# Kernel optimization log

Hardware: AMD Instinct MI355X
Metric: run time of the kernel (lower is better)

Reference implementation:

```python
import jax, jax.numpy as jnp
import numpy as np

D = 1024
H = 16

def setup_inputs() -> dict:
    key = jax.random.key(0)
    ks = jax.random.split(key, 5)
    x = jax.random.normal(ks[0], (2, 2048, D), dtype=jnp.float32)
    s = 0.02
    W_attn = jax.random.normal(ks[1], (D, 3 * D), dtype=jnp.float32) * s
    b_attn = jnp.zeros((3 * D,), dtype=jnp.float32)
    W_proj = jax.random.normal(ks[2], (D, D), dtype=jnp.float32) * s
    b_proj = jnp.zeros((D,), dtype=jnp.float32)
    return {"x": x, "W_attn": W_attn, "b_attn": b_attn, "W_proj": W_proj, "b_proj": b_proj}

def reference(x, W_attn, b_attn, W_proj, b_proj):
    B, S, E = x.shape
    hd = E // H  # head dim
    qkv = x @ W_attn + b_attn  # [B,S,3E]
    q, k, v = jnp.split(qkv, 3, axis=-1)
    # [B,S,E] -> [B,H,S,hd]
    q = q.reshape(B, S, H, hd).transpose(0, 2, 1, 3)
    k = k.reshape(B, S, H, hd).transpose(0, 2, 1, 3)
    v = v.reshape(B, S, H, hd).transpose(0, 2, 1, 3)
    att = jnp.einsum('bhqd,bhkd->bhqk', q, k) * (1.0 / jnp.sqrt(jnp.float32(hd)))
    causal = jnp.tril(jnp.ones((S, S), dtype=bool))
    att = jnp.where(causal, att, -jnp.inf)
    att = jax.nn.softmax(att, axis=-1)
    y = jnp.einsum('bhqk,bhkd->bhqd', att, v)
    y = y.transpose(0, 2, 1, 3).reshape(B, S, E)
    return y @ W_proj + b_proj
```

## Files before the change

kernel.cpp:

```cpp
#include <hip/hip_runtime.h>
#include <hip/hip_bf16.h>
#include <stdint.h>


typedef __attribute__((ext_vector_type(4))) float  f32x4;
typedef __attribute__((ext_vector_type(8))) __bf16 bf16x8;
typedef __attribute__((ext_vector_type(4))) short  s16x4;
typedef __attribute__((ext_vector_type(8))) short  s16x8;

#define MFMA(a, b, c) __builtin_amdgcn_mfma_f32_16x16x32_bf16((a), (b), (c), 0, 0, 0)

#if defined(__HIP_DEVICE_COMPILE__)
#define MFMA16(a, b, c) __builtin_amdgcn_mfma_f32_16x16x16bf16_1k((a), (b), (c), 0, 0, 0)
#else
#define MFMA16(a, b, c) (c)
#endif

__device__ __forceinline__ short f2bf(float x) {
#if defined(__HIP_DEVICE_COMPILE__)
  union { __bf16 b; short s; } u; u.b = (__bf16)x; return u.s;
#else
  union { float f; unsigned u; } v; v.f = x;
  unsigned r = v.u + 0x7FFFu + ((v.u >> 16) & 1u);
  return (short)(r >> 16);
#endif
}

__device__ __forceinline__ void gload16(const void* gptr, void* lptr) {
  __builtin_amdgcn_global_load_lds(
      (const __attribute__((address_space(1))) void*)gptr,
      (__attribute__((address_space(3))) void*)lptr, 16, 0, 0);
}


__global__ __launch_bounds__(256) void k_f32_to_bf16(const float* __restrict__ in,
                                                     short* __restrict__ out, int n) {
  int i = (blockIdx.x * 256 + threadIdx.x) * 4;
  if (i >= n) return;
  float4 v = *(const float4*)(in + i);
  s16x4 o;
  o[0] = f2bf(v.x); o[1] = f2bf(v.y); o[2] = f2bf(v.z); o[3] = f2bf(v.w);
  *(s16x4*)(out + i) = o;
}

__global__ __launch_bounds__(256) void k_transpose_bf(const float* __restrict__ W,
                                                      short* __restrict__ Wt, int R, int C) {
  __shared__ float tile[32][33];
  const int tx = threadIdx.x & 31, ty = threadIdx.x >> 5;
  const int bx = blockIdx.x * 32, by = blockIdx.y * 32;
#pragma unroll
  for (int i = 0; i < 4; ++i)
    tile[ty + i * 8][tx] = W[(long)(by + ty + i * 8) * C + bx + tx];
  __syncthreads();
#pragma unroll
  for (int i = 0; i < 4; ++i)
    Wt[(long)(bx + ty + i * 8) * R + by + tx] = f2bf(tile[tx][ty + i * 8]);
}


template <int EPI>
__global__ __launch_bounds__(256) void k_gemm(const short* __restrict__ A,
                                              const short* __restrict__ Bt,
                                              const float* __restrict__ bias,
                                              int M, int N, int K,
                                              short* __restrict__ q_out,
                                              short* __restrict__ k_out,
                                              short* __restrict__ vt_out,
                                              float* __restrict__ c_out) {
  __shared__ short As[3][4096];
  __shared__ short Bs[3][4096];
  const int tid  = threadIdx.x;
  const int lane = tid & 63;
  const int wave = tid >> 6;
  const int wm = (wave >> 1) * 64, wn = (wave & 1) * 64;
  const int bm = blockIdx.y * 128, bn = blockIdx.x * 128;
  const int sr = tid >> 2, sc = (tid & 3) * 8;
  const short* Ag = A + (long)(bm + sr) * K + sc;
  const short* Bg = Bt + (long)(bn + sr) * K + sc;
  const int fr = lane & 15, fg = lane >> 4;

  f32x4 acc[4][4];
#pragma unroll
  for (int i = 0; i < 4; ++i)
#pragma unroll
    for (int j = 0; j < 4; ++j) acc[i][j] = (f32x4){0.f, 0.f, 0.f, 0.f};

  auto stage = [&](int buf, int kt) {
    gload16(Ag + kt, &As[buf][tid * 8]);
    gload16(Ag + kt + 64 * K, &As[buf][2048 + tid * 8]);
    gload16(Bg + kt, &Bs[buf][tid * 8]);
    gload16(Bg + kt + 64 * K, &Bs[buf][2048 + tid * 8]);
  };
  auto compute = [&](int buf) {
    bf16x8 af[4], bfr[4];
    const short* Ar = &As[buf][(wm + fr) * 32 + fg * 8];
    const short* Br = &Bs[buf][(wn + fr) * 32 + fg * 8];
#pragma unroll
    for (int mi = 0; mi < 4; ++mi) af[mi] = *(const bf16x8*)(Ar + mi * 16 * 32);
#pragma unroll
    for (int ni = 0; ni < 4; ++ni) bfr[ni] = *(const bf16x8*)(Br + ni * 16 * 32);
#pragma unroll
    for (int mi = 0; mi < 4; ++mi)
#pragma unroll
      for (int ni = 0; ni < 4; ++ni)
        acc[mi][ni] = MFMA(af[mi], bfr[ni], acc[mi][ni]);
  };

  const int NT = K >> 5;
  stage(0, 0);
  stage(1, 32);
  for (int t = 0; t < NT - 1; ++t) {
    asm volatile("s_waitcnt vmcnt(4)" ::: "memory");
    __builtin_amdgcn_s_barrier();
    asm volatile("" ::: "memory");
    if (t + 2 < NT) stage((t + 2) % 3, (t + 2) << 5);
    compute(t % 3);
  }
  asm volatile("s_waitcnt vmcnt(0)" ::: "memory");
  __builtin_amdgcn_s_barrier();
  asm volatile("" ::: "memory");
  compute((NT - 1) % 3);

  const float QSC = 0.125f * 1.44269504088896341f;
#pragma unroll
  for (int mi = 0; mi < 4; ++mi) {
#pragma unroll
    for (int ni = 0; ni < 4; ++ni) {
      const int gcol  = bn + wn + ni * 16 + fr;
      const float bv  = bias[gcol];
      const int grow0 = bm + wm + mi * 16 + fg * 4;
      if (EPI == 0) {
        const int which = gcol >> 10;
        const int e = gcol & 1023;
        const int h = e >> 6, d = e & 63;
#pragma unroll
        for (int r = 0; r < 4; ++r) {
          const int mrow = grow0 + r;
          const int b = mrow >> 11, s = mrow & 2047;
          const float av = acc[mi][ni][r] + bv;
          if (which == 0)      q_out[((long)(b * 16 + h) * 2048 + s) * 64 + d] = f2bf(av * QSC);
          else if (which == 1) k_out[((long)(b * 16 + h) * 2048 + s) * 64 + d] = f2bf(av);
          else                 vt_out[((long)(b * 16 + h) * 64 + d) * 2048 + s] = f2bf(av);
        }
      } else {
#pragma unroll
        for (int r = 0; r < 4; ++r)
          c_out[(long)(grow0 + r) * N + gcol] = acc[mi][ni][r] + bv;
      }
    }
  }
}


__global__ __launch_bounds__(256, 4) void k_attn(const short* __restrict__ Qb,
                                                 const short* __restrict__ Kb,
                                                 const short* __restrict__ Vt,
                                                 short* __restrict__ Y) {
  __shared__ short smem[2][2][4096];
  const int bh = blockIdx.x;
  const int strip = 31 - blockIdx.y;
  const int qw0 = strip * 64;
  const int b = bh >> 4, h = bh & 15;
  const int tid = threadIdx.x;
  const int w = tid >> 6, lane = tid & 63;
  const int ql = lane & 15, g = lane >> 4;
  const short* Kp = Kb + (long)bh * 2048 * 64;
  const short* Vp = Vt + (long)bh * 64 * 2048;
  const short* Qp = Qb + ((long)bh * 2048 + qw0 + w * 16) * 64;

  const bf16x8 qf0 = *(const bf16x8*)(Qp + ql * 64 + g * 8);
  const bf16x8 qf1 = *(const bf16x8*)(Qp + ql * 64 + 32 + g * 8);

  const int sr_ = tid >> 3, sj_ = tid & 7;

  s16x4 ones;
  ones[0] = ones[1] = ones[2] = ones[3] = (short)0x3F80;

  f32x4 o[4];
#pragma unroll
  for (int df = 0; df < 4; ++df) o[df] = (f32x4){0.f, 0.f, 0.f, 0.f};
  f32x4 o_l = (f32x4){0.f, 0.f, 0.f, 0.f};
  float m = -1e30f;
  const int nt = strip + 1;

  {
#pragma unroll
    for (int j = 0; j < 2; ++j) {
      const int r = j * 32 + sr_;
      const int c = sj_ ^ (r & 7);
      gload16(Kp + (long)r * 64 + c * 8, &smem[0][0][j * 2048 + tid * 8]);
      gload16(Vp + (long)r * 2048 + c * 8, &smem[0][1][j * 2048 + tid * 8]);
    }
  }

  for (int t = 0; t < nt; ++t) {
    const int cur = t & 1;
    __syncthreads();
    if (t + 1 < nt) {
      const int k0n = (t + 1) * 64;
#pragma unroll
      for (int j = 0; j < 2; ++j) {
        const int r = j * 32 + sr_;
        const int c = sj_ ^ (r & 7);
        gload16(Kp + (long)(k0n + r) * 64 + c * 8, &smem[cur ^ 1][0][j * 2048 + tid * 8]);
        gload16(Vp + (long)r * 2048 + k0n + c * 8, &smem[cur ^ 1][1][j * 2048 + tid * 8]);
      }
    }
    const short* Kl = &smem[cur][0][0];
    const short* Vl = &smem[cur][1][0];
    const bool diag = (t == strip);

    float z[16];
    __builtin_amdgcn_s_setprio(1);
#pragma unroll
    for (int kf = 0; kf < 4; ++kf) {
      if (!diag || kf <= w) {
        const int r = kf * 16 + ql;
        const bf16x8 ka = *(const bf16x8*)(Kl + r * 64 + ((g ^ (r & 7)) * 8));
        const bf16x8 kb = *(const bf16x8*)(Kl + r * 64 + (((4 + g) ^ (r & 7)) * 8));
        f32x4 zz = (f32x4){0.f, 0.f, 0.f, 0.f};
        zz = MFMA(ka, qf0, zz);
        zz = MFMA(kb, qf1, zz);
        if (diag && kf == w) {
#pragma unroll
          for (int r4 = 0; r4 < 4; ++r4)
            z[kf * 4 + r4] = (g * 4 + r4 <= ql) ? zz[r4] : -3.0e38f;
        } else {
#pragma unroll
          for (int r4 = 0; r4 < 4; ++r4) z[kf * 4 + r4] = zz[r4];
        }
      } else {
#pragma unroll
        for (int r4 = 0; r4 < 4; ++r4) z[kf * 4 + r4] = -3.0e38f;
      }
    }
    __builtin_amdgcn_s_setprio(0);

    const float t1 = fmaxf(fmaxf(z[0], z[1]), z[2]);
    const float t2 = fmaxf(fmaxf(z[3], z[4]), z[5]);
    const float t3 = fmaxf(fmaxf(z[6], z[7]), z[8]);
    const float t4 = fmaxf(fmaxf(z[9], z[10]), z[11]);
    const float t5 = fmaxf(fmaxf(z[12], z[13]), z[14]);
    float tz = fmaxf(fmaxf(fmaxf(t1, t2), t3), fmaxf(fmaxf(t4, t5), z[15]));
    tz = fmaxf(tz, __shfl_xor(tz, 16));
    tz = fmaxf(tz, __shfl_xor(tz, 32));
    if (!__all(tz <= m + 8.0f)) {
      const float nm = fmaxf(m, tz);
      const float fac = exp2f(m - nm);
#pragma unroll
      for (int df = 0; df < 4; ++df) o[df] *= fac;
      o_l *= fac;
      m = nm;
    }
    __builtin_amdgcn_s_setprio(1);
#pragma unroll
    for (int kf = 0; kf < 4; ++kf) {
      if (!diag || kf <= w) {
        s16x4 pk;
        pk[0] = f2bf(exp2f(z[kf * 4 + 0] - m));
        pk[1] = f2bf(exp2f(z[kf * 4 + 1] - m));
        pk[2] = f2bf(exp2f(z[kf * 4 + 2] - m));
        pk[3] = f2bf(exp2f(z[kf * 4 + 3] - m));
        o_l = MFMA16(ones, pk, o_l);
#pragma unroll
        for (int df = 0; df < 4; ++df) {
          const int d = df * 16 + ql;
          const int c = kf * 2 + (g >> 1);
          const s16x4 vk = *(const s16x4*)(Vl + d * 64 + ((c ^ (d & 7)) * 8) + (g & 1) * 4);
          o[df] = MFMA16(vk, pk, o[df]);
        }
      }
    }
    __builtin_amdgcn_s_setprio(0);
  }

  __syncthreads();
  float* ot = (float*)&smem[0][0][0] + w * 1040;
  const float linv = 1.f / o_l[0];
#pragma unroll
  for (int df = 0; df < 4; ++df)
#pragma unroll
    for (int r = 0; r < 4; ++r)
      ot[ql * 65 + df * 16 + g * 4 + r] = o[df][r] * linv;
  const int q2 = lane >> 2, c4 = (lane & 3) * 16;
  short* Yp = Y + ((long)(b * 2048 + qw0 + w * 16 + q2)) * 1024 + h * 64 + c4;
  s16x8 y0, y1;
#pragma unroll
  for (int j = 0; j < 8; ++j) {
    y0[j] = f2bf(ot[q2 * 65 + c4 + j]);
    y1[j] = f2bf(ot[q2 * 65 + c4 + 8 + j]);
  }
  *(s16x8*)Yp = y0;
  *((s16x8*)(Yp + 8)) = y1;
}


extern "C" void kernel_launch(void* const* d_in, const int* in_sizes, int n_in,
                              void* d_out, int out_size, void* d_ws, size_t ws_size,
                              hipStream_t stream) {
  const float* x      = (const float*)d_in[0];
  const float* W_attn = (const float*)d_in[1];
  const float* b_attn = (const float*)d_in[2];
  const float* W_proj = (const float*)d_in[3];
  const float* b_proj = (const float*)d_in[4];
  float* out = (float*)d_out;

  char* ws = (char*)d_ws;
  short* x_bf = (short*)(ws);
  short* Wt_a = (short*)(ws + 8388608);
  short* Wt_p = (short*)(ws + 14680064);
  short* Qb   = (short*)(ws + 16777216);
  short* Kb   = (short*)(ws + 25165824);
  short* Vtb  = (short*)(ws + 33554432);
  short* y_bf = (short*)(ws + 41943040);

  k_f32_to_bf16<<<4096, 256, 0, stream>>>(x, x_bf, 4194304);
  k_transpose_bf<<<dim3(96, 32), 256, 0, stream>>>(W_attn, Wt_a, 1024, 3072);
  k_transpose_bf<<<dim3(32, 32), 256, 0, stream>>>(W_proj, Wt_p, 1024, 1024);
  k_gemm<0><<<dim3(24, 32), 256, 0, stream>>>(x_bf, Wt_a, b_attn, 4096, 3072, 1024,
                                              Qb, Kb, Vtb, nullptr);
  k_attn<<<dim3(32, 32), 256, 0, stream>>>(Qb, Kb, Vtb, y_bf);
  k_gemm<1><<<dim3(8, 32), 256, 0, stream>>>(y_bf, Wt_p, b_proj, 4096, 1024, 1024,
                                             nullptr, nullptr, nullptr, out);
}
```

Baseline: 127.7 us.

## Add 256x256-tile 8-wave QKV GEMM with phased double-buffered loads

Replaces the generic 128x128 QKV projection GEMM with a dedicated kernel that uses 256x256 tiles, 512 threads (8 waves), and a double-buffered LDS pipeline. Each 64-wide K step is split into four phases that interleave the next tile's half-loads with MFMA compute and raise wave priority around the MFMAs. The aim is more operand reuse per LDS byte and better overlap of global loads with compute. The cost is only 192 blocks, which may underfill the CUs, plus more registers and LDS per block. The output projection keeps the old kernel under a new name.

```diff
diff --git a/kernel.cpp b/kernel.cpp
--- a/kernel.cpp
+++ b/kernel.cpp
@@ -58,15 +58,118 @@
 }
 
 
-template <int EPI>
-__global__ __launch_bounds__(256) void k_gemm(const short* __restrict__ A,
-                                              const short* __restrict__ Bt,
-                                              const float* __restrict__ bias,
-                                              int M, int N, int K,
-                                              short* __restrict__ q_out,
-                                              short* __restrict__ k_out,
-                                              short* __restrict__ vt_out,
-                                              float* __restrict__ c_out) {
+#define QKV_PHASE(PH, KK, MIH, TAILVM)                                        \
+  {                                                                           \
+    if (t + 1 < NT) {                                                         \
+      stage_half(nxt, (PH), (t + 1) << 6);                                    \
+      asm volatile("s_waitcnt vmcnt(6)" ::: "memory");                        \
+    } else {                                                                  \
+      asm volatile("s_waitcnt vmcnt(" TAILVM ")" ::: "memory");               \
+    }                                                                         \
+    __builtin_amdgcn_s_barrier();                                             \
+    {                                                                         \
+      const short* Ab = &Als[cur][(KK) * 8192 + (wr * 128 + (MIH) * 64 + fr) * 32 + fg * 8]; \
+      if ((MIH) == 0) {                                                       \
+        const short* Bb = &Bls[cur][(KK) * 8192 + (wc * 64 + fr) * 32 + fg * 8]; \
+        _Pragma("unroll")                                                     \
+        for (int ni = 0; ni < 4; ++ni) bfr[ni] = *(const bf16x8*)(Bb + ni * 512); \
+      }                                                                       \
+      bf16x8 af[4];                                                           \
+      _Pragma("unroll")                                                       \
+      for (int mi = 0; mi < 4; ++mi) af[mi] = *(const bf16x8*)(Ab + mi * 512); \
+      __builtin_amdgcn_s_setprio(1);                                          \
+      _Pragma("unroll")                                                       \
+      for (int mi = 0; mi < 4; ++mi)                                          \
+        _Pragma("unroll")                                                     \
+        for (int ni = 0; ni < 4; ++ni)                                        \
+          acc[(MIH) * 4 + mi][ni] = MFMA(af[mi], bfr[ni], acc[(MIH) * 4 + mi][ni]); \
+      __builtin_amdgcn_s_setprio(0);                                          \
+    }                                                                         \
+  }
+
+__global__ __launch_bounds__(512, 2) void k_gemm_qkv(const short* __restrict__ A,
+                                                     const short* __restrict__ Bt,
+                                                     const float* __restrict__ bias,
+                                                     short* __restrict__ q_out,
+                                                     short* __restrict__ k_out,
+                                                     short* __restrict__ vt_out) {
+  constexpr int K = 1024;
+  constexpr int NT = 16;
+  __shared__ short Als[2][16384];
+  __shared__ short Bls[2][16384];
+  const int tid = threadIdx.x;
+  const int lane = tid & 63;
+  const int w = tid >> 6;
+  const int wr = w >> 2, wc = w & 3;
+  const int bm = blockIdx.y * 256, bn = blockIdx.x * 256;
+  const int fr = lane & 15, fg = lane >> 4;
+  const short* Ag = A + (long)(bm + (tid >> 2)) * K + (tid & 3) * 8;
+  const short* Bg = Bt + (long)(bn + (tid >> 2)) * K + (tid & 3) * 8;
+
+  f32x4 acc[8][4];
+#pragma unroll
+  for (int i = 0; i < 8; ++i)
+#pragma unroll
+    for (int j = 0; j < 4; ++j) acc[i][j] = (f32x4){0.f, 0.f, 0.f, 0.f};
+
+  auto stage_half = [&](int buf, int p, int kt) {
+    const int kk = p >> 1;
+    const int off = kt + kk * 32;
+    if (p & 1) {
+      short* dst = &Bls[buf][kk * 8192 + tid * 8];
+      gload16(Bg + off, dst);
+      gload16(Bg + 128 * K + off, dst + 4096);
+    } else {
+      short* dst = &Als[buf][kk * 8192 + tid * 8];
+      gload16(Ag + off, dst);
+      gload16(Ag + 128 * K + off, dst + 4096);
+    }
+  };
+
+  stage_half(0, 0, 0);
+  stage_half(0, 1, 0);
+  stage_half(0, 2, 0);
+  stage_half(0, 3, 0);
+
+  bf16x8 bfr[4];
+  for (int t = 0; t < NT; ++t) {
+    const int cur = t & 1, nxt = cur ^ 1;
+    QKV_PHASE(0, 0, 0, "6")
+    QKV_PHASE(1, 0, 1, "4")
+    QKV_PHASE(2, 1, 0, "2")
+    QKV_PHASE(3, 1, 1, "0")
+  }
+
+  const float QSC = 0.125f * 1.44269504088896341f;
+  const int which = bn >> 10;
+#pragma unroll
+  for (int mi = 0; mi < 8; ++mi) {
+#pragma unroll
+    for (int ni = 0; ni < 4; ++ni) {
+      const int gcol = bn + wc * 64 + ni * 16 + fr;
+      const float bv = bias[gcol];
+      const int grow0 = bm + wr * 128 + mi * 16 + fg * 4;
+      const int e = gcol & 1023;
+      const int h = e >> 6, d = e & 63;
+#pragma unroll
+      for (int r = 0; r < 4; ++r) {
+        const int mrow = grow0 + r;
+        const int b = mrow >> 11, s = mrow & 2047;
+        const float av = acc[mi][ni][r] + bv;
+        if (which == 0)      q_out[((long)(b * 16 + h) * 2048 + s) * 64 + d] = f2bf(av * QSC);
+        else if (which == 1) k_out[((long)(b * 16 + h) * 2048 + s) * 64 + d] = f2bf(av);
+        else                 vt_out[((long)(b * 16 + h) * 64 + d) * 2048 + s] = f2bf(av);
+      }
+    }
+  }
+}
+
+
+__global__ __launch_bounds__(256) void k_gemm_proj(const short* __restrict__ A,
+                                                   const short* __restrict__ Bt,
+                                                   const float* __restrict__ bias,
+                                                   int M, int N, int K,
+                                                   float* __restrict__ c_out) {
   __shared__ short As[3][4096];
   __shared__ short Bs[3][4096];
   const int tid  = threadIdx.x;
@@ -121,7 +224,6 @@
   asm volatile("" ::: "memory");
   compute((NT - 1) % 3);
 
-  const float QSC = 0.125f * 1.44269504088896341f;
 #pragma unroll
   for (int mi = 0; mi < 4; ++mi) {
 #pragma unroll
@@ -129,24 +231,9 @@
       const int gcol  = bn + wn + ni * 16 + fr;
       const float bv  = bias[gcol];
       const int grow0 = bm + wm + mi * 16 + fg * 4;
-      if (EPI == 0) {
-        const int which = gcol >> 10;
-        const int e = gcol & 1023;
-        const int h = e >> 6, d = e & 63;
-#pragma unroll
-        for (int r = 0; r < 4; ++r) {
-          const int mrow = grow0 + r;
-          const int b = mrow >> 11, s = mrow & 2047;
-          const float av = acc[mi][ni][r] + bv;
-          if (which == 0)      q_out[((long)(b * 16 + h) * 2048 + s) * 64 + d] = f2bf(av * QSC);
-          else if (which == 1) k_out[((long)(b * 16 + h) * 2048 + s) * 64 + d] = f2bf(av);
-          else                 vt_out[((long)(b * 16 + h) * 64 + d) * 2048 + s] = f2bf(av);
-        }
-      } else {
-#pragma unroll
-        for (int r = 0; r < 4; ++r)
-          c_out[(long)(grow0 + r) * N + gcol] = acc[mi][ni][r] + bv;
-      }
+#pragma unroll
+      for (int r = 0; r < 4; ++r)
+        c_out[(long)(grow0 + r) * N + gcol] = acc[mi][ni][r] + bv;
     }
   }
 }
@@ -317,9 +404,7 @@
   k_f32_to_bf16<<<4096, 256, 0, stream>>>(x, x_bf, 4194304);
   k_transpose_bf<<<dim3(96, 32), 256, 0, stream>>>(W_attn, Wt_a, 1024, 3072);
   k_transpose_bf<<<dim3(32, 32), 256, 0, stream>>>(W_proj, Wt_p, 1024, 1024);
-  k_gemm<0><<<dim3(24, 32), 256, 0, stream>>>(x_bf, Wt_a, b_attn, 4096, 3072, 1024,
-                                              Qb, Kb, Vtb, nullptr);
+  k_gemm_qkv<<<dim3(12, 16), 512, 0, stream>>>(x_bf, Wt_a, b_attn, Qb, Kb, Vtb);
   k_attn<<<dim3(32, 32), 256, 0, stream>>>(Qb, Kb, Vtb, y_bf);
-  k_gemm<1><<<dim3(8, 32), 256, 0, stream>>>(y_bf, Wt_p, b_proj, 4096, 1024, 1024,
-                                             nullptr, nullptr, nullptr, out);
-}
+  k_gemm_proj<<<dim3(8, 32), 256, 0, stream>>>(y_bf, Wt_p, b_proj, 4096, 1024, 1024, out);
+}
```

Result: slower. 145.6 us (+14.0%).

## Replace QKV GEMM with 256x256-tile 8-wave kernel using swizzled LDS

Applied to the files above, without the earlier changes.

The QKV projection moves from a 128x128-tile, 4-wave, triple-buffered GEMM to a dedicated 256x256-tile kernel with 8 waves and 64-wide K steps. It uses XOR-swizzled LDS layouts, double buffering with staggered A/B prefetch interleaved into the compute phases, and s_setprio around the MFMA bursts. The larger tile increases operand reuse per LDS load. In exchange it launches only 192 blocks, fewer than the 256 CUs, so it risks low occupancy and tail underuse, and the extra barriers per K step may add stalls.

```diff
diff --git a/kernel.cpp b/kernel.cpp
--- a/kernel.cpp
+++ b/kernel.cpp
@@ -58,15 +58,120 @@
 }
 
 
-template <int EPI>
-__global__ __launch_bounds__(256) void k_gemm(const short* __restrict__ A,
-                                              const short* __restrict__ Bt,
-                                              const float* __restrict__ bias,
-                                              int M, int N, int K,
-                                              short* __restrict__ q_out,
-                                              short* __restrict__ k_out,
-                                              short* __restrict__ vt_out,
-                                              float* __restrict__ c_out) {
+#define QKV_COMPUTE(KK, MIH, DOSTAGE)                                          \
+  {                                                                            \
+    if ((MIH) == 0) {                                                          \
+      _Pragma("unroll")                                                        \
+      for (int ni = 0; ni < 4; ++ni) {                                         \
+        const int row = wc * 64 + ni * 16 + fr;                                \
+        bfr[ni] = *(const bf16x8*)&Bls[cur][row * 64 + ((((KK)*4 + fg) ^ (fr & 7)) * 8)]; \
+      }                                                                        \
+    }                                                                          \
+    bf16x8 af[4];                                                              \
+    _Pragma("unroll")                                                          \
+    for (int mi = 0; mi < 4; ++mi) {                                           \
+      const int row = wr * 128 + (MIH) * 64 + mi * 16 + fr;                    \
+      af[mi] = *(const bf16x8*)&Als[cur][row * 64 + ((((KK)*4 + fg) ^ (fr & 7)) * 8)]; \
+    }                                                                          \
+    DOSTAGE;                                                                   \
+    __builtin_amdgcn_s_setprio(1);                                             \
+    _Pragma("unroll")                                                          \
+    for (int mi = 0; mi < 4; ++mi)                                             \
+      _Pragma("unroll")                                                        \
+      for (int ni = 0; ni < 4; ++ni)                                           \
+        acc[(MIH)*4 + mi][ni] = MFMA(af[mi], bfr[ni], acc[(MIH)*4 + mi][ni]);  \
+    __builtin_amdgcn_s_setprio(0);                                             \
+  }
+
+__global__ __launch_bounds__(512, 1) void k_gemm_qkv(const short* __restrict__ A,
+                                                     const short* __restrict__ Bt,
+                                                     const float* __restrict__ bias,
+                                                     short* __restrict__ q_out,
+                                                     short* __restrict__ k_out,
+                                                     short* __restrict__ vt_out) {
+  constexpr int K = 1024;
+  constexpr int NT = 16;
+  __shared__ short Als[2][16384];
+  __shared__ short Bls[2][16384];
+  const int tid = threadIdx.x;
+  const int lane = tid & 63;
+  const int w = tid >> 6;
+  const int wr = w >> 2, wc = w & 3;
+  const int bm = blockIdx.y * 256, bn = blockIdx.x * 256;
+  const int fr = lane & 15, fg = lane >> 4;
+
+  const int rt = tid >> 3;
+  const int csw = ((tid & 7) ^ (rt & 7)) * 8;
+  const short* Agb = A + (long)(bm + rt) * K + csw;
+  const short* Bgb = Bt + (long)(bn + rt) * K + csw;
+
+  f32x4 acc[8][4];
+#pragma unroll
+  for (int i = 0; i < 8; ++i)
+#pragma unroll
+    for (int j = 0; j < 4; ++j) acc[i][j] = (f32x4){0.f, 0.f, 0.f, 0.f};
+
+  auto stageA = [&](int buf, int t1) {
+    const long kt = (long)t1 << 6;
+#pragma unroll
+    for (int q = 0; q < 4; ++q)
+      gload16(Agb + kt + (long)q * (64 * K), &Als[buf][q * 4096 + tid * 8]);
+  };
+  auto stageB = [&](int buf, int t1) {
+    const long kt = (long)t1 << 6;
+#pragma unroll
+    for (int q = 0; q < 4; ++q)
+      gload16(Bgb + kt + (long)q * (64 * K), &Bls[buf][q * 4096 + tid * 8]);
+  };
+
+  stageA(0, 0);
+  stageB(0, 0);
+
+  bf16x8 bfr[4];
+  for (int t = 0; t < NT; ++t) {
+    const int cur = t & 1, nxt = cur ^ 1;
+    const bool pre = (t + 1 < NT);
+    asm volatile("s_waitcnt vmcnt(0)" ::: "memory");
+    __builtin_amdgcn_s_barrier();
+    QKV_COMPUTE(0, 0, { if (pre) stageA(nxt, t + 1); })
+    __builtin_amdgcn_s_barrier();
+    QKV_COMPUTE(0, 1, {})
+    __builtin_amdgcn_s_barrier();
+    QKV_COMPUTE(1, 0, { if (pre) stageB(nxt, t + 1); })
+    __builtin_amdgcn_s_barrier();
+    QKV_COMPUTE(1, 1, {})
+  }
+
+  const float QSC = 0.125f * 1.44269504088896341f;
+  const int which = bn >> 10;
+#pragma unroll
+  for (int mi = 0; mi < 8; ++mi) {
+#pragma unroll
+    for (int ni = 0; ni < 4; ++ni) {
+      const int gcol = bn + wc * 64 + ni * 16 + fr;
+      const float bv = bias[gcol];
+      const int grow0 = bm + wr * 128 + mi * 16 + fg * 4;
+      const int e = gcol & 1023;
+      const int h = e >> 6, d = e & 63;
+#pragma unroll
+      for (int r = 0; r < 4; ++r) {
+        const int mrow = grow0 + r;
+        const int b = mrow >> 11, s = mrow & 2047;
+        const float av = acc[mi][ni][r] + bv;
+        if (which == 0)      q_out[((long)(b * 16 + h) * 2048 + s) * 64 + d] = f2bf(av * QSC);
+        else if (which == 1) k_out[((long)(b * 16 + h) * 2048 + s) * 64 + d] = f2bf(av);
+        else                 vt_out[((long)(b * 16 + h) * 64 + d) * 2048 + s] = f2bf(av);
+      }
+    }
+  }
+}
+
+
+__global__ __launch_bounds__(256) void k_gemm_proj(const short* __restrict__ A,
+                                                   const short* __restrict__ Bt,
+                                                   const float* __restrict__ bias,
+                                                   int M, int N, int K,
+                                                   float* __restrict__ c_out) {
   __shared__ short As[3][4096];
   __shared__ short Bs[3][4096];
   const int tid  = threadIdx.x;
@@ -121,7 +226,6 @@
   asm volatile("" ::: "memory");
   compute((NT - 1) % 3);
 
-  const float QSC = 0.125f * 1.44269504088896341f;
 #pragma unroll
   for (int mi = 0; mi < 4; ++mi) {
 #pragma unroll
@@ -129,24 +233,9 @@
       const int gcol  = bn + wn + ni * 16 + fr;
       const float bv  = bias[gcol];
       const int grow0 = bm + wm + mi * 16 + fg * 4;
-      if (EPI == 0) {
-        const int which = gcol >> 10;
-        const int e = gcol & 1023;
-        const int h = e >> 6, d = e & 63;
-#pragma unroll
-        for (int r = 0; r < 4; ++r) {
-          const int mrow = grow0 + r;
-          const int b = mrow >> 11, s = mrow & 2047;
-          const float av = acc[mi][ni][r] + bv;
-          if (which == 0)      q_out[((long)(b * 16 + h) * 2048 + s) * 64 + d] = f2bf(av * QSC);
-          else if (which == 1) k_out[((long)(b * 16 + h) * 2048 + s) * 64 + d] = f2bf(av);
-          else                 vt_out[((long)(b * 16 + h) * 64 + d) * 2048 + s] = f2bf(av);
-        }
-      } else {
-#pragma unroll
-        for (int r = 0; r < 4; ++r)
-          c_out[(long)(grow0 + r) * N + gcol] = acc[mi][ni][r] + bv;
-      }
+#pragma unroll
+      for (int r = 0; r < 4; ++r)
+        c_out[(long)(grow0 + r) * N + gcol] = acc[mi][ni][r] + bv;
     }
   }
 }
@@ -317,9 +406,7 @@
   k_f32_to_bf16<<<4096, 256, 0, stream>>>(x, x_bf, 4194304);
   k_transpose_bf<<<dim3(96, 32), 256, 0, stream>>>(W_attn, Wt_a, 1024, 3072);
   k_transpose_bf<<<dim3(32, 32), 256, 0, stream>>>(W_proj, Wt_p, 1024, 1024);
-  k_gemm<0><<<dim3(24, 32), 256, 0, stream>>>(x_bf, Wt_a, b_attn, 4096, 3072, 1024,
-                                              Qb, Kb, Vtb, nullptr);
+  k_gemm_qkv<<<dim3(12, 16), 512, 0, stream>>>(x_bf, Wt_a, b_attn, Qb, Kb, Vtb);
   k_attn<<<dim3(32, 32), 256, 0, stream>>>(Qb, Kb, Vtb, y_bf);
-  k_gemm<1><<<dim3(8, 32), 256, 0, stream>>>(y_bf, Wt_p, b_proj, 4096, 1024, 1024,
-                                             nullptr, nullptr, nullptr, out);
-}
+  k_gemm_proj<<<dim3(8, 32), 256, 0, stream>>>(y_bf, Wt_p, b_proj, 4096, 1024, 1024, out);
+}
```

New measurement: 143.5 us. 1.12x slower.

## Process two 16-row query blocks per wave in attention; fuse prep kernels

Applied to the files above, without the earlier changes.

Each attention wave now handles 32 query rows (two 16-row groups) instead of 16, so each K/V tile loaded into LDS is reused across a 128-row strip and the grid shrinks to 32x16 blocks. Causal masking is generalized per sub-block using diagonal offsets, and occupancy is relaxed to 2 blocks per SM to allow more registers. Separately, the bf16 conversion of x and the two weight transposes are merged into one launch to cut launch overhead. The trade-offs are higher register pressure, fewer blocks in flight, and a coarser causal load imbalance.

```diff
diff --git a/kernel.cpp b/kernel.cpp
--- a/kernel.cpp
+++ b/kernel.cpp
@@ -33,21 +33,33 @@
 }
 
 
-__global__ __launch_bounds__(256) void k_f32_to_bf16(const float* __restrict__ in,
-                                                     short* __restrict__ out, int n) {
-  int i = (blockIdx.x * 256 + threadIdx.x) * 4;
-  if (i >= n) return;
-  float4 v = *(const float4*)(in + i);
-  s16x4 o;
-  o[0] = f2bf(v.x); o[1] = f2bf(v.y); o[2] = f2bf(v.z); o[3] = f2bf(v.w);
-  *(s16x4*)(out + i) = o;
-}
-
-__global__ __launch_bounds__(256) void k_transpose_bf(const float* __restrict__ W,
-                                                      short* __restrict__ Wt, int R, int C) {
+__global__ __launch_bounds__(256) void k_prep(const float* __restrict__ x,
+                                              const float* __restrict__ Wa,
+                                              const float* __restrict__ Wp,
+                                              short* __restrict__ x_bf,
+                                              short* __restrict__ Wt_a,
+                                              short* __restrict__ Wt_p) {
   __shared__ float tile[32][33];
+  const int id = blockIdx.x;
+  if (id < 4096) {
+    const int i = (id * 256 + threadIdx.x) * 4;
+    float4 v = *(const float4*)(x + i);
+    s16x4 o;
+    o[0] = f2bf(v.x); o[1] = f2bf(v.y); o[2] = f2bf(v.z); o[3] = f2bf(v.w);
+    *(s16x4*)(x_bf + i) = o;
+    return;
+  }
+  const float* W; short* Wt; int R, C, bx, by;
+  if (id < 7168) {
+    const int id2 = id - 4096;
+    W = Wa; Wt = Wt_a; R = 1024; C = 3072;
+    bx = (id2 % 96) * 32; by = (id2 / 96) * 32;
+  } else {
+    const int id2 = id - 7168;
+    W = Wp; Wt = Wt_p; R = 1024; C = 1024;
+    bx = (id2 & 31) * 32; by = (id2 >> 5) * 32;
+  }
   const int tx = threadIdx.x & 31, ty = threadIdx.x >> 5;
-  const int bx = blockIdx.x * 32, by = blockIdx.y * 32;
 #pragma unroll
   for (int i = 0; i < 4; ++i)
     tile[ty + i * 8][tx] = W[(long)(by + ty + i * 8) * C + bx + tx];
@@ -152,36 +164,39 @@
 }
 
 
-__global__ __launch_bounds__(256, 4) void k_attn(const short* __restrict__ Qb,
+__global__ __launch_bounds__(256, 2) void k_attn(const short* __restrict__ Qb,
                                                  const short* __restrict__ Kb,
                                                  const short* __restrict__ Vt,
                                                  short* __restrict__ Y) {
   __shared__ short smem[2][2][4096];
   const int bh = blockIdx.x;
-  const int strip = 31 - blockIdx.y;
-  const int qw0 = strip * 64;
+  const int strip = 15 - blockIdx.y;
+  const int qw0 = strip * 128;
   const int b = bh >> 4, h = bh & 15;
   const int tid = threadIdx.x;
   const int w = tid >> 6, lane = tid & 63;
   const int ql = lane & 15, g = lane >> 4;
   const short* Kp = Kb + (long)bh * 2048 * 64;
   const short* Vp = Vt + (long)bh * 64 * 2048;
-  const short* Qp = Qb + ((long)bh * 2048 + qw0 + w * 16) * 64;
-
-  const bf16x8 qf0 = *(const bf16x8*)(Qp + ql * 64 + g * 8);
-  const bf16x8 qf1 = *(const bf16x8*)(Qp + ql * 64 + 32 + g * 8);
+  const int qb0 = qw0 + w * 32;
+  const short* Qp = Qb + ((long)bh * 2048 + qb0) * 64;
+
+  const bf16x8 qf0a = *(const bf16x8*)(Qp + ql * 64 + g * 8);
+  const bf16x8 qf0b = *(const bf16x8*)(Qp + ql * 64 + 32 + g * 8);
+  const bf16x8 qf1a = *(const bf16x8*)(Qp + (16 + ql) * 64 + g * 8);
+  const bf16x8 qf1b = *(const bf16x8*)(Qp + (16 + ql) * 64 + 32 + g * 8);
 
   const int sr_ = tid >> 3, sj_ = tid & 7;
 
   s16x4 ones;
   ones[0] = ones[1] = ones[2] = ones[3] = (short)0x3F80;
 
-  f32x4 o[4];
-#pragma unroll
-  for (int df = 0; df < 4; ++df) o[df] = (f32x4){0.f, 0.f, 0.f, 0.f};
-  f32x4 o_l = (f32x4){0.f, 0.f, 0.f, 0.f};
-  float m = -1e30f;
-  const int nt = strip + 1;
+  f32x4 o0[4], o1[4];
+#pragma unroll
+  for (int df = 0; df < 4; ++df) { o0[df] = (f32x4){0.f,0.f,0.f,0.f}; o1[df] = (f32x4){0.f,0.f,0.f,0.f}; }
+  f32x4 ol0 = (f32x4){0.f,0.f,0.f,0.f}, ol1 = (f32x4){0.f,0.f,0.f,0.f};
+  float m0 = -1e30f, m1 = -1e30f;
+  const int nt = 2 * strip + 2;
 
   {
 #pragma unroll
@@ -208,66 +223,101 @@
     }
     const short* Kl = &smem[cur][0][0];
     const short* Vl = &smem[cur][1][0];
-    const bool diag = (t == strip);
-
-    float z[16];
+    const int k0 = t * 64;
+    const int dq0 = (qb0 - k0) >> 4;
+    const int dq1 = dq0 + 1;
+
+    float z0[16], z1[16];
+#pragma unroll
+    for (int j = 0; j < 16; ++j) { z0[j] = -3.0e38f; z1[j] = -3.0e38f; }
     __builtin_amdgcn_s_setprio(1);
 #pragma unroll
     for (int kf = 0; kf < 4; ++kf) {
-      if (!diag || kf <= w) {
+      if (kf <= dq1) {
         const int r = kf * 16 + ql;
         const bf16x8 ka = *(const bf16x8*)(Kl + r * 64 + ((g ^ (r & 7)) * 8));
         const bf16x8 kb = *(const bf16x8*)(Kl + r * 64 + (((4 + g) ^ (r & 7)) * 8));
-        f32x4 zz = (f32x4){0.f, 0.f, 0.f, 0.f};
-        zz = MFMA(ka, qf0, zz);
-        zz = MFMA(kb, qf1, zz);
-        if (diag && kf == w) {
-#pragma unroll
-          for (int r4 = 0; r4 < 4; ++r4)
-            z[kf * 4 + r4] = (g * 4 + r4 <= ql) ? zz[r4] : -3.0e38f;
-        } else {
-#pragma unroll
-          for (int r4 = 0; r4 < 4; ++r4) z[kf * 4 + r4] = zz[r4];
-        }
-      } else {
-#pragma unroll
-        for (int r4 = 0; r4 < 4; ++r4) z[kf * 4 + r4] = -3.0e38f;
+        if (kf <= dq0) {
+          f32x4 zz = (f32x4){0.f, 0.f, 0.f, 0.f};
+          zz = MFMA(ka, qf0a, zz);
+          zz = MFMA(kb, qf0b, zz);
+          if (kf == dq0) {
+#pragma unroll
+            for (int r4 = 0; r4 < 4; ++r4)
+              z0[kf * 4 + r4] = (g * 4 + r4 <= ql) ? zz[r4] : -3.0e38f;
+          } else {
+#pragma unroll
+            for (int r4 = 0; r4 < 4; ++r4) z0[kf * 4 + r4] = zz[r4];
+          }
+        }
+        {
+          f32x4 zz = (f32x4){0.f, 0.f, 0.f, 0.f};
+          zz = MFMA(ka, qf1a, zz);
+          zz = MFMA(kb, qf1b, zz);
+          if (kf == dq1) {
+#pragma unroll
+            for (int r4 = 0; r4 < 4; ++r4)
+              z1[kf * 4 + r4] = (g * 4 + r4 <= ql) ? zz[r4] : -3.0e38f;
+          } else {
+#pragma unroll
+            for (int r4 = 0; r4 < 4; ++r4) z1[kf * 4 + r4] = zz[r4];
+          }
+        }
       }
     }
     __builtin_amdgcn_s_setprio(0);
 
-    const float t1 = fmaxf(fmaxf(z[0], z[1]), z[2]);
-    const float t2 = fmaxf(fmaxf(z[3], z[4]), z[5]);
-    const float t3 = fmaxf(fmaxf(z[6], z[7]), z[8]);
-    const float t4 = fmaxf(fmaxf(z[9], z[10]), z[11]);
-    const float t5 = fmaxf(fmaxf(z[12], z[13]), z[14]);
-    float tz = fmaxf(fmaxf(fmaxf(t1, t2), t3), fmaxf(fmaxf(t4, t5), z[15]));
-    tz = fmaxf(tz, __shfl_xor(tz, 16));
-    tz = fmaxf(tz, __shfl_xor(tz, 32));
-    if (!__all(tz <= m + 8.0f)) {
-      const float nm = fmaxf(m, tz);
-      const float fac = exp2f(m - nm);
-#pragma unroll
-      for (int df = 0; df < 4; ++df) o[df] *= fac;
-      o_l *= fac;
-      m = nm;
+    const float a1 = fmaxf(fmaxf(z0[0], z0[1]), z0[2]);
+    const float a2 = fmaxf(fmaxf(z0[3], z0[4]), z0[5]);
+    const float a3 = fmaxf(fmaxf(z0[6], z0[7]), z0[8]);
+    const float a4 = fmaxf(fmaxf(z0[9], z0[10]), z0[11]);
+    const float a5 = fmaxf(fmaxf(z0[12], z0[13]), z0[14]);
+    float tz0 = fmaxf(fmaxf(fmaxf(a1, a2), a3), fmaxf(fmaxf(a4, a5), z0[15]));
+    const float c1 = fmaxf(fmaxf(z1[0], z1[1]), z1[2]);
+    const float c2 = fmaxf(fmaxf(z1[3], z1[4]), z1[5]);
+    const float c3 = fmaxf(fmaxf(z1[6], z1[7]), z1[8]);
+    const float c4_ = fmaxf(fmaxf(z1[9], z1[10]), z1[11]);
+    const float c5 = fmaxf(fmaxf(z1[12], z1[13]), z1[14]);
+    float tz1 = fmaxf(fmaxf(fmaxf(c1, c2), c3), fmaxf(fmaxf(c4_, c5), z1[15]));
+    tz0 = fmaxf(tz0, __shfl_xor(tz0, 16));
+    tz0 = fmaxf(tz0, __shfl_xor(tz0, 32));
+    tz1 = fmaxf(tz1, __shfl_xor(tz1, 16));
+    tz1 = fmaxf(tz1, __shfl_xor(tz1, 32));
+    if (!__all(tz0 <= m0 + 8.0f && tz1 <= m1 + 8.0f)) {
+      const float nm0 = fmaxf(m0, tz0);
+      const float fac0 = exp2f(m0 - nm0);
+      const float nm1 = fmaxf(m1, tz1);
+      const float fac1 = exp2f(m1 - nm1);
+#pragma unroll
+      for (int df = 0; df < 4; ++df) { o0[df] *= fac0; o1[df] *= fac1; }
+      ol0 *= fac0; ol1 *= fac1;
+      m0 = nm0; m1 = nm1;
     }
     __builtin_amdgcn_s_setprio(1);
 #pragma unroll
     for (int kf = 0; kf < 4; ++kf) {
-      if (!diag || kf <= w) {
-        s16x4 pk;
-        pk[0] = f2bf(exp2f(z[kf * 4 + 0] - m));
-        pk[1] = f2bf(exp2f(z[kf * 4 + 1] - m));
-        pk[2] = f2bf(exp2f(z[kf * 4 + 2] - m));
-        pk[3] = f2bf(exp2f(z[kf * 4 + 3] - m));
-        o_l = MFMA16(ones, pk, o_l);
+      if (kf <= dq1) {
+        const bool g0 = (kf <= dq0);
+        s16x4 pk0, pk1;
+        if (g0) {
+          pk0[0] = f2bf(exp2f(z0[kf * 4 + 0] - m0));
+          pk0[1] = f2bf(exp2f(z0[kf * 4 + 1] - m0));
+          pk0[2] = f2bf(exp2f(z0[kf * 4 + 2] - m0));
+          pk0[3] = f2bf(exp2f(z0[kf * 4 + 3] - m0));
+          ol0 = MFMA16(ones, pk0, ol0);
+        }
+        pk1[0] = f2bf(exp2f(z1[kf * 4 + 0] - m1));
+        pk1[1] = f2bf(exp2f(z1[kf * 4 + 1] - m1));
+        pk1[2] = f2bf(exp2f(z1[kf * 4 + 2] - m1));
+        pk1[3] = f2bf(exp2f(z1[kf * 4 + 3] - m1));
+        ol1 = MFMA16(ones, pk1, ol1);
 #pragma unroll
         for (int df = 0; df < 4; ++df) {
           const int d = df * 16 + ql;
           const int c = kf * 2 + (g >> 1);
           const s16x4 vk = *(const s16x4*)(Vl + d * 64 + ((c ^ (d & 7)) * 8) + (g & 1) * 4);
-          o[df] = MFMA16(vk, pk, o[df]);
+          if (g0) o0[df] = MFMA16(vk, pk0, o0[df]);
+          o1[df] = MFMA16(vk, pk1, o1[df]);
         }
       }
     }
@@ -276,22 +326,41 @@
 
   __syncthreads();
   float* ot = (float*)&smem[0][0][0] + w * 1040;
-  const float linv = 1.f / o_l[0];
+  const int q2 = lane >> 2, c4 = (lane & 3) * 16;
+  const float linv0 = 1.f / ol0[0];
 #pragma unroll
   for (int df = 0; df < 4; ++df)
 #pragma unroll
     for (int r = 0; r < 4; ++r)
-      ot[ql * 65 + df * 16 + g * 4 + r] = o[df][r] * linv;
-  const int q2 = lane >> 2, c4 = (lane & 3) * 16;
-  short* Yp = Y + ((long)(b * 2048 + qw0 + w * 16 + q2)) * 1024 + h * 64 + c4;
-  s16x8 y0, y1;
-#pragma unroll
-  for (int j = 0; j < 8; ++j) {
-    y0[j] = f2bf(ot[q2 * 65 + c4 + j]);
-    y1[j] = f2bf(ot[q2 * 65 + c4 + 8 + j]);
-  }
-  *(s16x8*)Yp = y0;
-  *((s16x8*)(Yp + 8)) = y1;
+      ot[ql * 65 + df * 16 + g * 4 + r] = o0[df][r] * linv0;
+  {
+    short* Yp = Y + ((long)(b * 2048 + qb0 + q2)) * 1024 + h * 64 + c4;
+    s16x8 y0, y1;
+#pragma unroll
+    for (int j = 0; j < 8; ++j) {
+      y0[j] = f2bf(ot[q2 * 65 + c4 + j]);
+      y1[j] = f2bf(ot[q2 * 65 + c4 + 8 + j]);
+    }
+    *(s16x8*)Yp = y0;
+    *((s16x8*)(Yp + 8)) = y1;
+  }
+  const float linv1 = 1.f / ol1[0];
+#pragma unroll
+  for (int df = 0; df < 4; ++df)
+#pragma unroll
+    for (int r = 0; r < 4; ++r)
+      ot[ql * 65 + df * 16 + g * 4 + r] = o1[df][r] * linv1;
+  {
+    short* Yp = Y + ((long)(b * 2048 + qb0 + 16 + q2)) * 1024 + h * 64 + c4;
+    s16x8 y0, y1;
+#pragma unroll
+    for (int j = 0; j < 8; ++j) {
+      y0[j] = f2bf(ot[q2 * 65 + c4 + j]);
+      y1[j] = f2bf(ot[q2 * 65 + c4 + 8 + j]);
+    }
+    *(s16x8*)Yp = y0;
+    *((s16x8*)(Yp + 8)) = y1;
+  }
 }
 
 
@@ -314,12 +383,10 @@
   short* Vtb  = (short*)(ws + 33554432);
   short* y_bf = (short*)(ws + 41943040);
 
-  k_f32_to_bf16<<<4096, 256, 0, stream>>>(x, x_bf, 4194304);
-  k_transpose_bf<<<dim3(96, 32), 256, 0, stream>>>(W_attn, Wt_a, 1024, 3072);
-  k_transpose_bf<<<dim3(32, 32), 256, 0, stream>>>(W_proj, Wt_p, 1024, 1024);
+  k_prep<<<8192, 256, 0, stream>>>(x, W_attn, W_proj, x_bf, Wt_a, Wt_p);
   k_gemm<0><<<dim3(24, 32), 256, 0, stream>>>(x_bf, Wt_a, b_attn, 4096, 3072, 1024,
                                               Qb, Kb, Vtb, nullptr);
-  k_attn<<<dim3(32, 32), 256, 0, stream>>>(Qb, Kb, Vtb, y_bf);
+  k_attn<<<dim3(32, 16), 256, 0, stream>>>(Qb, Kb, Vtb, y_bf);
   k_gemm<1><<<dim3(8, 32), 256, 0, stream>>>(y_bf, Wt_p, b_proj, 4096, 1024, 1024,
                                              nullptr, nullptr, nullptr, out);
 }
```

Result: slower. 167.9 us (+31.4%).
